# Kernel tuning notes

Measured on AMD Instinct MI355X. Metric: run time of the kernel, lower is better.

## Reference

```python
import jax, jax.numpy as jnp
import numpy as np

B, L, D, H, BS, R, MLP = 2, 4096, 768, 12, 64, 3, 3072
HD = D // H            # 64 head dim
NB = L // BS           # 64 blocks
EPS = 1e-6
SEED = 0               # connectivity_seed


def _rand_plan():
    """Static BigBird key-block plan for middle query blocks: [NB-2, 5+R].
    Columns: global first, global last, window (i-1, i, i+1), R random blocks."""
    rng = np.random.RandomState(SEED)
    rows = []
    for i in range(1, NB - 1):
        excl = {0, NB - 1, i - 1, i, i + 1}
        cand = np.array([j for j in range(NB) if j not in excl])
        rnd = rng.choice(cand, size=R, replace=False)
        rows.append(np.concatenate([np.array([0, NB - 1, i - 1, i, i + 1]), rnd]))
    return jnp.asarray(np.stack(rows), dtype=jnp.int32)

_PLAN = _rand_plan()


def _layernorm(x, scale, bias):
    mu = jnp.mean(x, axis=-1, keepdims=True)
    var = jnp.mean(jnp.square(x - mu), axis=-1, keepdims=True)
    return (x - mu) * jax.lax.rsqrt(var + EPS) * scale + bias


def _bigbird_attention(x, Wq, Wk, Wv, Wo):
    # projections: [B,L,D] x [D,H,HD] -> [B,H,L,HD]; flax scales q by 1/sqrt(HD)
    q = jnp.einsum('bld,dhk->bhlk', x, Wq) / jnp.sqrt(jnp.asarray(HD, x.dtype))
    k = jnp.einsum('bld,dhk->bhlk', x, Wk)
    v = jnp.einsum('bld,dhk->bhlk', x, Wv)
    qb = q.reshape(B, H, NB, BS, HD)
    kb = k.reshape(B, H, NB, BS, HD)
    vb = v.reshape(B, H, NB, BS, HD)
    # global query rows (first & last block) attend densely to all keys
    qg = qb[:, :, jnp.array([0, NB - 1])]                 # [B,H,2,BS,HD]
    sg = jnp.einsum('bhgqd,bhld->bhgql', qg, k)           # [B,H,2,BS,L]
    og = jnp.einsum('bhgql,bhld->bhgqd', jax.nn.softmax(sg, axis=-1), v)
    # middle query rows: gather window + global + random key blocks
    S = _PLAN.shape[1]                                     # 5 + R = 8 blocks
    km = kb[:, :, _PLAN].reshape(B, H, NB - 2, S * BS, HD)
    vm = vb[:, :, _PLAN].reshape(B, H, NB - 2, S * BS, HD)
    sm = jnp.einsum('bhmqd,bhmkd->bhmqk', qb[:, :, 1:NB - 1], km)
    om = jnp.einsum('bhmqk,bhmkd->bhmqd', jax.nn.softmax(sm, axis=-1), vm)
    ob = jnp.concatenate([og[:, :, :1], om, og[:, :, 1:]], axis=2)  # [B,H,NB,BS,HD]
    o = ob.reshape(B, H, L, HD)
    return jnp.einsum('bhlk,hkd->bld', o, Wo)


def setup_inputs() -> dict:
    key = jax.random.key(0)
    ks = jax.random.split(key, 8)
    s_qkv = (2.0 / (D + HD)) ** 0.5   # xavier-uniform-ish std
    s_mlp1 = (2.0 / (D + MLP)) ** 0.5
    return {
        'x': jax.random.normal(ks[0], (B, L, D), jnp.float32),
        'ln1_scale': jnp.ones((D,), jnp.float32),
        'ln1_bias': jnp.zeros((D,), jnp.float32),
        'Wq': jax.random.normal(ks[1], (D, H, HD), jnp.float32) * s_qkv,
        'Wk': jax.random.normal(ks[2], (D, H, HD), jnp.float32) * s_qkv,
        'Wv': jax.random.normal(ks[3], (D, H, HD), jnp.float32) * s_qkv,
        'Wo': jax.random.normal(ks[4], (H, HD, D), jnp.float32) * s_qkv,
        'ln2_scale': jnp.ones((D,), jnp.float32),
        'ln2_bias': jnp.zeros((D,), jnp.float32),
        'W1': jax.random.normal(ks[5], (D, MLP), jnp.float32) * s_mlp1,
        'b1': jnp.zeros((MLP,), jnp.float32),
        'W2': jax.random.normal(ks[6], (MLP, D), jnp.float32) * s_mlp1,
        'b2': jnp.zeros((D,), jnp.float32),
    }


def reference(x, ln1_scale, ln1_bias, Wq, Wk, Wv, Wo, ln2_scale, ln2_bias, W1, b1, W2, b2):
    h = _layernorm(x, ln1_scale, ln1_bias)
    attn = _bigbird_attention(h, Wq, Wk, Wv, Wo)
    x1 = attn + x                                  # residual (dropout deterministic)
    y = _layernorm(x1, ln2_scale, ln2_bias)
    y = jax.nn.relu(jnp.einsum('bld,df->blf', y, W1) + b1)
    y = jnp.einsum('blf,fd->bld', y, W2) + b2
    return x1 + y
```

## Files before the change

### kernel.cpp

```cpp
#include <hip/hip_runtime.h>
#include <stdint.h>

constexpr int D_MODEL = 768;
constexpr int SEQ     = 4096;
constexpr int NHEAD   = 12;
constexpr int HDIM    = 64;
constexpr int BATCH   = 2;
constexpr int DFF     = 3072;
constexpr int ROWS    = BATCH * SEQ;

typedef __attribute__((ext_vector_type(8))) __bf16 bfrag;
typedef __attribute__((ext_vector_type(8))) short  s16x8;
typedef __attribute__((ext_vector_type(4))) float  f32x4;

#define MFMA16(a, b, c) __builtin_amdgcn_mfma_f32_16x16x32_bf16((a), (b), (c), 0, 0, 0)
#define AS1(p) ((__attribute__((address_space(1))) void*)(uintptr_t)(p))
#define AS3(p) ((__attribute__((address_space(3))) void*)(p))

__device__ __forceinline__ float b2f(short s) {
  union { unsigned u; float f; } c;
  c.u = ((unsigned)(unsigned short)s) << 16;
  return c.f;
}
__device__ __forceinline__ short f2b(float f) {
  union { float f; unsigned u; } c;
  c.f = f;
  unsigned r = c.u + 0x7fffu + ((c.u >> 16) & 1u);
  return (short)(r >> 16);
}

struct PlanT { int v[64][8]; };

struct MTRng {
  unsigned mt[624];
  int mti;
  constexpr MTRng() : mt{}, mti(624) {
    mt[0] = 0u;
    for (int i = 1; i < 624; ++i)
      mt[i] = 1812433253u * (mt[i-1] ^ (mt[i-1] >> 30)) + (unsigned)i;
  }
  constexpr unsigned next() {
    if (mti >= 624) {
      for (int i = 0; i < 624; ++i) {
        unsigned y = (mt[i] & 0x80000000u) | (mt[(i+1) % 624] & 0x7fffffffu);
        unsigned v = mt[(i+397) % 624] ^ (y >> 1);
        if (y & 1u) v ^= 0x9908b0dfu;
        mt[i] = v;
      }
      mti = 0;
    }
    unsigned y = mt[mti++];
    y ^= y >> 11;
    y ^= (y << 7)  & 0x9d2c5680u;
    y ^= (y << 15) & 0xefc60000u;
    y ^= y >> 18;
    return y;
  }
  constexpr unsigned interval(unsigned mx) {
    unsigned mask = mx;
    mask |= mask >> 1; mask |= mask >> 2; mask |= mask >> 4;
    mask |= mask >> 8; mask |= mask >> 16;
    unsigned v = next() & mask;
    while (v > mx) v = next() & mask;
    return v;
  }
};

constexpr PlanT make_plan() {
  PlanT P{};
  MTRng rng{};
  for (int i = 1; i <= 62; ++i) {
    int cand[64] = {}; int n = 0;
    for (int j = 0; j < 64; ++j) {
      if (j == 0 || j == 63 || j == i-1 || j == i || j == i+1) continue;
      cand[n++] = j;
    }
    int perm[64] = {};
    for (int p = 0; p < n; ++p) perm[p] = p;
    for (int p = n - 1; p > 0; --p) {
      int j = (int)rng.interval((unsigned)p);
      int t = perm[p]; perm[p] = perm[j]; perm[j] = t;
    }
    P.v[i][0] = 0;  P.v[i][1] = 63; P.v[i][2] = i-1; P.v[i][3] = i; P.v[i][4] = i+1;
    P.v[i][5] = cand[perm[0]]; P.v[i][6] = cand[perm[1]]; P.v[i][7] = cand[perm[2]];
  }
  return P;
}
constexpr PlanT h_plan = make_plan();
__constant__ PlanT g_plan = h_plan;

__global__ __launch_bounds__(256) void ln_kernel(
    const float* __restrict__ x, const float* __restrict__ sc,
    const float* __restrict__ bi, short* __restrict__ y)
{
  const int row = blockIdx.x, tid = threadIdx.x;
  const size_t base = (size_t)row * D_MODEL;
  float v0 = x[base + tid], v1 = x[base + tid + 256], v2 = x[base + tid + 512];
  float s  = v0 + v1 + v2;
  float s2 = v0*v0 + v1*v1 + v2*v2;
  for (int off = 1; off < 64; off <<= 1) {
    s  += __shfl_xor(s,  off);
    s2 += __shfl_xor(s2, off);
  }
  __shared__ float red[8];
  if ((tid & 63) == 0) { red[tid >> 6] = s; red[4 + (tid >> 6)] = s2; }
  __syncthreads();
  s  = red[0] + red[1] + red[2] + red[3];
  s2 = red[4] + red[5] + red[6] + red[7];
  const float mu  = s * (1.f / 768.f);
  const float var = s2 * (1.f / 768.f) - mu * mu;
  const float rs  = rsqrtf(var + 1e-6f);
  short* yr = y + base;
  yr[tid]       = f2b((v0 - mu) * rs * sc[tid]       + bi[tid]);
  yr[tid + 256] = f2b((v1 - mu) * rs * sc[tid + 256] + bi[tid + 256]);
  yr[tid + 512] = f2b((v2 - mu) * rs * sc[tid + 512] + bi[tid + 512]);
}

struct TrArgs { const float* src[6]; short* dst[6]; };

__global__ __launch_bounds__(256) void tr_all(TrArgs a) {
  __shared__ short tile[32][33];
  const int idx = blockIdx.x;
  int w, bx, by, Rr, Cc;
  if (idx < 2304)      { w = idx / 576; int t = idx % 576;  bx = t % 24; by = t / 24; Rr = 768;  Cc = 768;  }
  else if (idx < 4608) { w = 4;         int t = idx - 2304; bx = t % 96; by = t / 96; Rr = 768;  Cc = 3072; }
  else                 { w = 5;         int t = idx - 4608; bx = t % 24; by = t / 24; Rr = 3072; Cc = 768;  }
  const float* in = a.src[w];
  short* out = a.dst[w];
  const int x0 = bx * 32, y0 = by * 32;
  const int tx = threadIdx.x & 31, ty = threadIdx.x >> 5;
  for (int i = 0; i < 32; i += 8)
    tile[ty + i][tx] = f2b(in[(size_t)(y0 + ty + i) * Cc + x0 + tx]);
  __syncthreads();
  for (int i = 0; i < 32; i += 8)
    out[(size_t)(x0 + ty + i) * Rr + y0 + tx] = tile[tx][ty + i];
}

enum { M_QKV = 0, M_RES = 3, M_BRELU = 4, M_BRES = 5 };

template <int MODE, int TN>
__global__ __launch_bounds__(256) void gemm_bt(
    const short* __restrict__ A, const short* __restrict__ Bt,
    void* __restrict__ Cv, short* __restrict__ C2, short* __restrict__ C3,
    const float* __restrict__ res, const float* __restrict__ bias, int N, int K)
{
  constexpr int NT = TN / 32;
  alignas(16) __shared__ short As[128 * 32];
  alignas(16) __shared__ short Bs[TN * 32];
  const int tid = threadIdx.x;
  const int wave = tid >> 6, lane = tid & 63;
  const int quad = lane >> 4, l15 = lane & 15;
  const int m0 = blockIdx.x * 128, n0 = blockIdx.y * TN;
  const int mw = (wave & 1) * 64, nw = (wave >> 1) * (TN / 2);

  f32x4 acc[4][NT];
#pragma unroll
  for (int i = 0; i < 4; ++i)
#pragma unroll
    for (int j = 0; j < NT; ++j) acc[i][j] = f32x4{0.f, 0.f, 0.f, 0.f};

  const int srow = wave * 32 + (lane >> 2);
  const int scol = (lane & 3) * 8;
  const size_t arow = (size_t)(m0 + srow) * K + scol;
  const size_t brow128 = (size_t)(n0 + srow) * K + scol;
  const size_t brow64  = (size_t)(n0 + wave * 16 + (lane >> 2)) * K + scol;

  for (int k0 = 0; k0 < K; k0 += 32) {
    __syncthreads();
    __builtin_amdgcn_global_load_lds(AS1(A + arow + k0),                AS3(As + (wave*32     ) * 32), 16, 0, 0);
    __builtin_amdgcn_global_load_lds(AS1(A + arow + k0 + (size_t)16*K), AS3(As + (wave*32 + 16) * 32), 16, 0, 0);
    if constexpr (TN == 128) {
      __builtin_amdgcn_global_load_lds(AS1(Bt + brow128 + k0),                AS3(Bs + (wave*32     ) * 32), 16, 0, 0);
      __builtin_amdgcn_global_load_lds(AS1(Bt + brow128 + k0 + (size_t)16*K), AS3(Bs + (wave*32 + 16) * 32), 16, 0, 0);
    } else {
      __builtin_amdgcn_global_load_lds(AS1(Bt + brow64 + k0), AS3(Bs + (wave*16) * 32), 16, 0, 0);
    }
    __syncthreads();
    bfrag af[4], bfv[NT];
#pragma unroll
    for (int mt = 0; mt < 4; ++mt)  af[mt]  = *(const bfrag*)(As + (mw + mt*16 + l15) * 32 + quad * 8);
#pragma unroll
    for (int nt = 0; nt < NT; ++nt) bfv[nt] = *(const bfrag*)(Bs + (nw + nt*16 + l15) * 32 + quad * 8);
#pragma unroll
    for (int mt = 0; mt < 4; ++mt)
#pragma unroll
      for (int nt = 0; nt < NT; ++nt)
        acc[mt][nt] = MFMA16(af[mt], bfv[nt], acc[mt][nt]);
  }

#pragma unroll
  for (int mt = 0; mt < 4; ++mt) {
#pragma unroll
    for (int nt = 0; nt < NT; ++nt) {
#pragma unroll
      for (int r = 0; r < 4; ++r) {
        const int gm = m0 + mw + mt*16 + quad*4 + r;
        const int gn = n0 + nw + nt*16 + l15;
        float v = acc[mt][nt][r];
        if (MODE == M_QKV) {
          const int seg = gn / 768, gn2 = gn - seg * 768;
          if (seg == 0)      ((short*)Cv)[(size_t)gm * 768 + gn2] = f2b(v * 0.125f);
          else if (seg == 1) C2[(size_t)gm * 768 + gn2] = f2b(v);
          else {
            const int bb = gm >> 12, l = gm & 4095, hh = gn2 >> 6, hd = gn2 & 63;
            C3[(((size_t)(bb * NHEAD + hh)) * HDIM + hd) * SEQ + l] = f2b(v);
          }
        } else {
          const size_t ci = (size_t)gm * N + gn;
          if (MODE == M_RES)   { ((float*)Cv)[ci] = v + res[ci]; }
          if (MODE == M_BRELU) { v += bias[gn]; ((short*)Cv)[ci] = f2b(v > 0.f ? v : 0.f); }
          if (MODE == M_BRES)  { ((float*)Cv)[ci] = v + bias[gn] + res[ci]; }
        }
      }
    }
  }
}

constexpr int PSTR = 72;
constexpr int KSTR = 68;

__global__ __launch_bounds__(256, 3) void attn_kernel(
    const short* __restrict__ q, const short* __restrict__ k,
    const short* __restrict__ vt, short* __restrict__ o,
    short* __restrict__ Opart, float* __restrict__ ml)
{
  alignas(16) __shared__ short KV[4][64 * KSTR];
  alignas(16) __shared__ short Pbuf[4][2 * 16 * PSTR];
  const int xi = blockIdx.x, h = blockIdx.y, b = blockIdx.z;
  const int tid = threadIdx.x, wave = tid >> 6, lane = tid & 63;
  const int quad = lane >> 4, l15 = lane & 15;
  const int r8 = lane >> 3, g8 = lane & 7;

  int qb, part = 0, g = 0;
  bool partial;
  if (xi < 62) { qb = xi + 1; partial = false; }
  else { const int t = xi - 62; g = t >> 3; part = t & 7; qb = g ? 63 : 0; partial = true; }

  const short* qp = q + (size_t)(b * SEQ + qb * 64 + wave * 16 + l15) * D_MODEL + h * HDIM;
  const bfrag qf0 = *(const bfrag*)(qp + quad * 8);
  const bfrag qf1 = *(const bfrag*)(qp + 32 + quad * 8);

  const short* kb_base = k  + (size_t)b * SEQ * D_MODEL + h * HDIM;
  const short* vt_base = vt + ((size_t)(b * NHEAD + h)) * HDIM * SEQ;

  const int sr0 = wave * 16 + r8, sr1 = wave * 16 + 8 + r8;

  auto kidx = [&](int t, int which) -> int {
    const int tt = t > 3 ? 3 : t;
    return partial ? (part * 8 + 2 * tt + which) : g_plan.v[qb][2 * tt + which];
  };
  auto load8 = [&](int k0i, int k1i, s16x8* R) {
    const short* ka = kb_base + (size_t)k0i * 64 * D_MODEL + g8 * 8;
    const short* kbp = kb_base + (size_t)k1i * 64 * D_MODEL + g8 * 8;
    const short* va = vt_base + (size_t)k0i * 64 + g8 * 8;
    const short* vb = vt_base + (size_t)k1i * 64 + g8 * 8;
    R[0] = *(const s16x8*)(ka  + (size_t)sr0 * D_MODEL);
    R[1] = *(const s16x8*)(ka  + (size_t)sr1 * D_MODEL);
    R[2] = *(const s16x8*)(kbp + (size_t)sr0 * D_MODEL);
    R[3] = *(const s16x8*)(kbp + (size_t)sr1 * D_MODEL);
    R[4] = *(const s16x8*)(va  + (size_t)sr0 * SEQ);
    R[5] = *(const s16x8*)(va  + (size_t)sr1 * SEQ);
    R[6] = *(const s16x8*)(vb  + (size_t)sr0 * SEQ);
    R[7] = *(const s16x8*)(vb  + (size_t)sr1 * SEQ);
  };

  float m_r[4], l_r[4];
  f32x4 oacc[4];
#pragma unroll
  for (int r = 0; r < 4; ++r) { m_r[r] = -1e9f; l_r[r] = 0.f; }
#pragma unroll
  for (int nt = 0; nt < 4; ++nt) oacc[nt] = f32x4{0.f, 0.f, 0.f, 0.f};

  short* pb = &Pbuf[wave][0];

  s16x8 R[8];
  load8(kidx(0, 0), kidx(0, 1), R);

  for (int it = 0; it < 4; ++it) {
    __syncthreads();
#pragma unroll
    for (int bu = 0; bu < 4; ++bu) {
      *(s16x8*)(&KV[bu][sr0 * KSTR + g8 * 8]) = R[2 * bu];
      *(s16x8*)(&KV[bu][sr1 * KSTR + g8 * 8]) = R[2 * bu + 1];
    }
    __syncthreads();

    load8(kidx(it + 1, 0), kidx(it + 1, 1), R);

    f32x4 s0[4], s1[4];
#pragma unroll
    for (int nt = 0; nt < 4; ++nt) {
      const int fr = (nt * 16 + l15) * KSTR + quad * 8;
      const bfrag ka0 = *(const bfrag*)(&KV[0][fr]);
      const bfrag ka1 = *(const bfrag*)(&KV[0][fr + 32]);
      const bfrag kb0 = *(const bfrag*)(&KV[1][fr]);
      const bfrag kb1 = *(const bfrag*)(&KV[1][fr + 32]);
      s0[nt] = f32x4{0.f,0.f,0.f,0.f}; s1[nt] = f32x4{0.f,0.f,0.f,0.f};
      s0[nt] = MFMA16(qf0, ka0, s0[nt]); s0[nt] = MFMA16(qf1, ka1, s0[nt]);
      s1[nt] = MFMA16(qf0, kb0, s1[nt]); s1[nt] = MFMA16(qf1, kb1, s1[nt]);
    }

    float alpha[4];
#pragma unroll
    for (int r = 0; r < 4; ++r) {
      float v = fmaxf(fmaxf(fmaxf(s0[0][r], s0[1][r]), fmaxf(s0[2][r], s0[3][r])),
                      fmaxf(fmaxf(s1[0][r], s1[1][r]), fmaxf(s1[2][r], s1[3][r])));
      v = fmaxf(v, __shfl_xor(v, 1));
      v = fmaxf(v, __shfl_xor(v, 2));
      v = fmaxf(v, __shfl_xor(v, 4));
      v = fmaxf(v, __shfl_xor(v, 8));
      const float mn = fmaxf(m_r[r], v);
      alpha[r] = __expf(m_r[r] - mn);
      m_r[r] = mn;
    }
    float psum[4] = {0.f, 0.f, 0.f, 0.f};
#pragma unroll
    for (int nt = 0; nt < 4; ++nt)
#pragma unroll
      for (int r = 0; r < 4; ++r) {
        const float p0 = __expf(s0[nt][r] - m_r[r]);
        const float p1 = __expf(s1[nt][r] - m_r[r]);
        s0[nt][r] = p0; s1[nt][r] = p1;
        psum[r] += p0 + p1;
      }
#pragma unroll
    for (int r = 0; r < 4; ++r) {
      float v = psum[r];
      v += __shfl_xor(v, 1); v += __shfl_xor(v, 2);
      v += __shfl_xor(v, 4); v += __shfl_xor(v, 8);
      l_r[r] = l_r[r] * alpha[r] + v;
    }

#pragma unroll
    for (int nt = 0; nt < 4; ++nt)
#pragma unroll
      for (int r = 0; r < 4; ++r) {
        pb[(quad * 4 + r) * PSTR + nt * 16 + l15]             = f2b(s0[nt][r]);
        pb[16 * PSTR + (quad * 4 + r) * PSTR + nt * 16 + l15] = f2b(s1[nt][r]);
      }

#pragma unroll
    for (int nt = 0; nt < 4; ++nt)
#pragma unroll
      for (int r = 0; r < 4; ++r) oacc[nt][r] *= alpha[r];
#pragma unroll
    for (int s = 0; s < 2; ++s) {
      const bfrag pf0 = *(const bfrag*)(pb + l15 * PSTR + s * 32 + quad * 8);
      const bfrag pf1 = *(const bfrag*)(pb + 16 * PSTR + l15 * PSTR + s * 32 + quad * 8);
#pragma unroll
      for (int nt = 0; nt < 4; ++nt) {
        const int fr = (nt * 16 + l15) * KSTR + s * 32 + quad * 8;
        const bfrag vf0 = *(const bfrag*)(&KV[2][fr]);
        const bfrag vf1 = *(const bfrag*)(&KV[3][fr]);
        oacc[nt] = MFMA16(pf0, vf0, oacc[nt]);
        oacc[nt] = MFMA16(pf1, vf1, oacc[nt]);
      }
    }
  }

  if (!partial) {
    short* op = o + (size_t)(b * SEQ + qb * 64 + wave * 16) * D_MODEL + h * HDIM;
#pragma unroll
    for (int r = 0; r < 4; ++r) {
      const float inv = 1.f / l_r[r];
#pragma unroll
      for (int nt = 0; nt < 4; ++nt)
        op[(size_t)(quad * 4 + r) * D_MODEL + nt * 16 + l15] = f2b(oacc[nt][r] * inv);
    }
  } else {
    const int pi = ((b * NHEAD + h) * 2 + g) * 8 + part;
    short* Op = Opart + (size_t)pi * 4096;
    float* mp = ml + (size_t)pi * 128;
#pragma unroll
    for (int r = 0; r < 4; ++r) {
      const int row = wave * 16 + quad * 4 + r;
#pragma unroll
      for (int nt = 0; nt < 4; ++nt)
        Op[row * 64 + nt * 16 + l15] = f2b(oacc[nt][r]);
      if (l15 == 0) { mp[row] = m_r[r]; mp[64 + row] = l_r[r]; }
    }
  }
}

__global__ __launch_bounds__(256) void attn_merge(
    const short* __restrict__ Opart, const float* __restrict__ ml,
    short* __restrict__ o)
{
  const int bi = blockIdx.x;
  const int g = bi & 1, h = (bi >> 1) % NHEAD, b = bi / (2 * NHEAD);
  const int qb = g ? 63 : 0;
  const int pi0 = bi * 8;
#pragma unroll
  for (int e = 0; e < 16; ++e) {
    const int idx = threadIdx.x + e * 256;
    const int r = idx >> 6, c = idx & 63;
    float ms = -1e9f;
#pragma unroll
    for (int p = 0; p < 8; ++p) ms = fmaxf(ms, ml[(size_t)(pi0 + p) * 128 + r]);
    float lsum = 0.f, osum = 0.f;
#pragma unroll
    for (int p = 0; p < 8; ++p) {
      const float w = __expf(ml[(size_t)(pi0 + p) * 128 + r] - ms);
      lsum += w * ml[(size_t)(pi0 + p) * 128 + 64 + r];
      osum += w * b2f(Opart[(size_t)(pi0 + p) * 4096 + idx]);
    }
    o[(size_t)(b * SEQ + qb * 64 + r) * D_MODEL + h * HDIM + c] = f2b(osum / lsum);
  }
}

extern "C" void kernel_launch(void* const* d_in, const int* in_sizes, int n_in,
                              void* d_out, int out_size, void* d_ws, size_t ws_size,
                              hipStream_t stream) {
  (void)in_sizes; (void)n_in; (void)out_size; (void)ws_size;
  const float* x    = (const float*)d_in[0];
  const float* ln1s = (const float*)d_in[1];
  const float* ln1b = (const float*)d_in[2];
  const float* Wq   = (const float*)d_in[3];
  const float* Wk   = (const float*)d_in[4];
  const float* Wv   = (const float*)d_in[5];
  const float* Wo   = (const float*)d_in[6];
  const float* ln2s = (const float*)d_in[7];
  const float* ln2b = (const float*)d_in[8];
  const float* W1   = (const float*)d_in[9];
  const float* b1   = (const float*)d_in[10];
  const float* W2   = (const float*)d_in[11];
  const float* b2   = (const float*)d_in[12];
  float* out = (float*)d_out;

  short* WqT  = (short*)((char*)d_ws + 256);
  short* WkT  = WqT  + 768 * 768;
  short* WvT  = WkT  + 768 * 768;
  short* WoT  = WvT  + 768 * 768;
  short* W1T  = WoT  + 768 * 768;
  short* W2T  = W1T  + (size_t)3072 * 768;
  short* hbuf = W2T  + (size_t)3072 * 768;
  short* qbuf = hbuf + (size_t)ROWS * D_MODEL;
  short* kbuf = qbuf + (size_t)ROWS * D_MODEL;
  short* vtb  = kbuf + (size_t)ROWS * D_MODEL;
  short* obuf = vtb  + (size_t)ROWS * D_MODEL;
  short* tbuf = qbuf;
  short* Opart = hbuf;
  float* mlbuf = (float*)(hbuf + (size_t)384 * 4096);

  TrArgs ta;
  ta.src[0] = Wq; ta.src[1] = Wk; ta.src[2] = Wv; ta.src[3] = Wo; ta.src[4] = W1; ta.src[5] = W2;
  ta.dst[0] = WqT; ta.dst[1] = WkT; ta.dst[2] = WvT; ta.dst[3] = WoT; ta.dst[4] = W1T; ta.dst[5] = W2T;
  tr_all<<<6912, 256, 0, stream>>>(ta);

  ln_kernel<<<ROWS, 256, 0, stream>>>(x, ln1s, ln1b, hbuf);

  gemm_bt<M_QKV, 128><<<dim3(64, 18), 256, 0, stream>>>(hbuf, WqT, qbuf, kbuf, vtb, nullptr, nullptr, 2304, 768);

  attn_kernel<<<dim3(78, 12, 2), 256, 0, stream>>>(qbuf, kbuf, vtb, obuf, Opart, mlbuf);
  attn_merge<<<48, 256, 0, stream>>>(Opart, mlbuf, obuf);

  gemm_bt<M_RES, 64><<<dim3(64, 12), 256, 0, stream>>>(obuf, WoT, out, nullptr, nullptr, x, nullptr, 768, 768);

  ln_kernel<<<ROWS, 256, 0, stream>>>(out, ln2s, ln2b, hbuf);

  gemm_bt<M_BRELU, 128><<<dim3(64, 24), 256, 0, stream>>>(hbuf, W1T, tbuf, nullptr, nullptr, nullptr, b1, 3072, 768);
  gemm_bt<M_BRES, 64> <<<dim3(64, 12), 256, 0, stream>>>(tbuf, W2T, out, nullptr, nullptr, out, b2, 768, 3072);
}
```

Baseline: 392.9 us.

## Replace GEMMs with 256x256 multi-stage pipelined kernel and split-K atomic FFN2

```diff
diff --git a/kernel.cpp b/kernel.cpp
--- a/kernel.cpp
+++ b/kernel.cpp
@@ -27,6 +27,15 @@
   c.f = f;
   unsigned r = c.u + 0x7fffu + ((c.u >> 16) & 1u);
   return (short)(r >> 16);
+}
+
+__device__ __forceinline__ void atomAddF(float* p, float v) {
+#if __has_builtin(__builtin_amdgcn_global_atomic_fadd_f32)
+  (void)__builtin_amdgcn_global_atomic_fadd_f32(
+      (__attribute__((address_space(1))) float*)(uintptr_t)p, v);
+#else
+  atomicAdd(p, v);
+#endif
 }
 
 struct PlanT { int v[64][8]; };
@@ -136,68 +145,129 @@
     out[(size_t)(x0 + ty + i) * Rr + y0 + tx] = tile[tx][ty + i];
 }
 
-enum { M_QKV = 0, M_RES = 3, M_BRELU = 4, M_BRES = 5 };
-
-template <int MODE, int TN>
-__global__ __launch_bounds__(256) void gemm_bt(
+enum { M_QKV = 0, M_RES = 3, M_BRELU = 4, M_BRES_AT = 6 };
+
+template <int MODE>
+__global__ __launch_bounds__(512, 2) void gemm256(
     const short* __restrict__ A, const short* __restrict__ Bt,
     void* __restrict__ Cv, short* __restrict__ C2, short* __restrict__ C3,
-    const float* __restrict__ res, const float* __restrict__ bias, int N, int K)
+    const float* __restrict__ res, const float* __restrict__ bias,
+    int N, int K, int ksz)
 {
-  constexpr int NT = TN / 32;
-  alignas(16) __shared__ short As[128 * 32];
-  alignas(16) __shared__ short Bs[TN * 32];
-  const int tid = threadIdx.x;
-  const int wave = tid >> 6, lane = tid & 63;
+  alignas(16) __shared__ short KV[10 * 8192];
+  const int tid  = threadIdx.x;
+  const int wid  = tid >> 6, lane = tid & 63;
   const int quad = lane >> 4, l15 = lane & 15;
-  const int m0 = blockIdx.x * 128, n0 = blockIdx.y * TN;
-  const int mw = (wave & 1) * 64, nw = (wave >> 1) * (TN / 2);
-
-  f32x4 acc[4][NT];
-#pragma unroll
-  for (int i = 0; i < 4; ++i)
-#pragma unroll
-    for (int j = 0; j < NT; ++j) acc[i][j] = f32x4{0.f, 0.f, 0.f, 0.f};
-
-  const int srow = wave * 32 + (lane >> 2);
-  const int scol = (lane & 3) * 8;
-  const size_t arow = (size_t)(m0 + srow) * K + scol;
-  const size_t brow128 = (size_t)(n0 + srow) * K + scol;
-  const size_t brow64  = (size_t)(n0 + wave * 16 + (lane >> 2)) * K + scol;
-
-  for (int k0 = 0; k0 < K; k0 += 32) {
-    __syncthreads();
-    __builtin_amdgcn_global_load_lds(AS1(A + arow + k0),                AS3(As + (wave*32     ) * 32), 16, 0, 0);
-    __builtin_amdgcn_global_load_lds(AS1(A + arow + k0 + (size_t)16*K), AS3(As + (wave*32 + 16) * 32), 16, 0, 0);
-    if constexpr (TN == 128) {
-      __builtin_amdgcn_global_load_lds(AS1(Bt + brow128 + k0),                AS3(Bs + (wave*32     ) * 32), 16, 0, 0);
-      __builtin_amdgcn_global_load_lds(AS1(Bt + brow128 + k0 + (size_t)16*K), AS3(Bs + (wave*32 + 16) * 32), 16, 0, 0);
-    } else {
-      __builtin_amdgcn_global_load_lds(AS1(Bt + brow64 + k0), AS3(Bs + (wave*16) * 32), 16, 0, 0);
-    }
-    __syncthreads();
-    bfrag af[4], bfv[NT];
-#pragma unroll
-    for (int mt = 0; mt < 4; ++mt)  af[mt]  = *(const bfrag*)(As + (mw + mt*16 + l15) * 32 + quad * 8);
-#pragma unroll
-    for (int nt = 0; nt < NT; ++nt) bfv[nt] = *(const bfrag*)(Bs + (nw + nt*16 + l15) * 32 + quad * 8);
-#pragma unroll
-    for (int mt = 0; mt < 4; ++mt)
-#pragma unroll
-      for (int nt = 0; nt < NT; ++nt)
-        acc[mt][nt] = MFMA16(af[mt], bfv[nt], acc[mt][nt]);
-  }
-
-#pragma unroll
-  for (int mt = 0; mt < 4; ++mt) {
-#pragma unroll
-    for (int nt = 0; nt < NT; ++nt) {
+  const int wr = wid >> 2, wn = wid & 3, bh = wn >> 1;
+  const int m0 = blockIdx.x * 256, n0 = blockIdx.y * 256;
+  const int kbase = blockIdx.z * ksz;
+  const int NK = ksz >> 6;
+
+  const int rsub = tid >> 3;
+  const int scol = ((tid & 7) ^ (rsub & 7)) * 8;
+  const short* pa  = A  + (size_t)(m0 + rsub) * K + kbase + scol;
+  const short* pb  = Bt + (size_t)(n0 + rsub) * K + kbase + scol;
+  const short* pa1 = pa + (size_t)128 * K;
+  const short* pb1 = pb + (size_t)128 * K;
+
+#define STAGE(slot, src) do {                                                       \
+    short* _d = (short*)KV + (slot) * 8192 + wid * 512;                             \
+    __builtin_amdgcn_global_load_lds(AS1(src), AS3(_d), 16, 0, 0);                  \
+    __builtin_amdgcn_global_load_lds(AS1((src) + (size_t)64 * K), AS3(_d + 4096), 16, 0, 0); \
+  } while (0)
+
+  const int xorv  = (l15 & 7) << 4;
+  const int aoff0 = l15 * 128 + ((quad * 16) ^ xorv);
+  const int aoff1 = l15 * 128 + ((64 + quad * 16) ^ xorv);
+  const int boff0 = (wn & 1) * 8192 + aoff0;
+  const int boff1 = (wn & 1) * 8192 + aoff1;
+
+  f32x4 acc[8][4];
+#pragma unroll
+  for (int i = 0; i < 8; ++i)
+#pragma unroll
+    for (int j = 0; j < 4; ++j) acc[i][j] = f32x4{0.f, 0.f, 0.f, 0.f};
+
+  STAGE(0, pa);       STAGE(1, pa1);
+  STAGE(2, pb);       STAGE(3, pb1);
+  STAGE(4, pa + 64);  STAGE(5, pa1 + 64);
+  asm volatile("s_waitcnt vmcnt(4)" ::: "memory");
+  __builtin_amdgcn_s_barrier();
+  __builtin_amdgcn_sched_barrier(0);
+
+#define LDA(mtb) _Pragma("unroll")                                   \
+    for (int mi = 0; mi < 4; ++mi) {                                 \
+      af[mi][0] = *(const bfrag*)(Ab0 + ((mtb) + mi) * 2048);        \
+      af[mi][1] = *(const bfrag*)(Ab1 + ((mtb) + mi) * 2048); }
+#define LDB(ntb) _Pragma("unroll")                                   \
+    for (int ni = 0; ni < 2; ++ni) {                                 \
+      bf[ni][0] = *(const bfrag*)(Bb0 + ((ntb) + ni) * 2048);        \
+      bf[ni][1] = *(const bfrag*)(Bb1 + ((ntb) + ni) * 2048); }
+#define MM(mtb, ntb)                                                 \
+    __builtin_amdgcn_s_setprio(1);                                   \
+    _Pragma("unroll")                                                \
+    for (int mi = 0; mi < 4; ++mi)                                   \
+      _Pragma("unroll")                                              \
+      for (int ni = 0; ni < 2; ++ni) {                               \
+        acc[(mtb)+mi][(ntb)+ni] = MFMA16(af[mi][0], bf[ni][0], acc[(mtb)+mi][(ntb)+ni]); \
+        acc[(mtb)+mi][(ntb)+ni] = MFMA16(af[mi][1], bf[ni][1], acc[(mtb)+mi][(ntb)+ni]); \
+      }                                                              \
+    __builtin_amdgcn_s_setprio(0);
+
+  int s0 = 0;
+  for (int kt = 0; kt < NK; ++kt) {
+    int tA = s0 + wr;      const int sA = (tA >= 10) ? tA - 10 : tA;
+    int tB = s0 + 2 + bh;  const int sB = (tB >= 10) ? tB - 10 : tB;
+    const char* KB  = (const char*)KV;
+    const char* Ab0 = KB + sA * 16384 + aoff0;
+    const char* Ab1 = KB + sA * 16384 + aoff1;
+    const char* Bb0 = KB + sB * 16384 + boff0;
+    const char* Bb1 = KB + sB * 16384 + boff1;
+    int st0 = s0 + 6; if (st0 >= 10) st0 -= 10;
+    int st1 = st0 + 1; if (st1 >= 10) st1 -= 10;
+    int st2 = st1 + 1; if (st2 >= 10) st2 -= 10;
+    int st3 = st2 + 1; if (st3 >= 10) st3 -= 10;
+    int kkB = kt + 1; if (kkB >= NK) kkB = 0;
+    int kkA = kt + 2; if (kkA >= NK) kkA = 0;
+
+    bfrag af[4][2], bf[2][2];
+
+    LDB(0); LDA(0);
+    STAGE(st0, pb + kkB * 64);
+    MM(0, 0);
+    __builtin_amdgcn_sched_barrier(0);
+    LDB(2);
+    STAGE(st1, pb1 + kkB * 64);
+    MM(0, 2);
+    __builtin_amdgcn_sched_barrier(0);
+    LDA(4);
+    STAGE(st2, pa + kkA * 64);
+    MM(4, 2);
+    __builtin_amdgcn_sched_barrier(0);
+    LDB(0);
+    STAGE(st3, pa1 + kkA * 64);
+    MM(4, 0);
+    asm volatile("s_waitcnt vmcnt(4)" ::: "memory");
+    __builtin_amdgcn_s_barrier();
+    __builtin_amdgcn_sched_barrier(0);
+
+    s0 += 4; if (s0 >= 10) s0 -= 10;
+  }
+#undef LDA
+#undef LDB
+#undef MM
+#undef STAGE
+
+#pragma unroll
+  for (int mt = 0; mt < 8; ++mt) {
+#pragma unroll
+    for (int nt = 0; nt < 4; ++nt) {
 #pragma unroll
       for (int r = 0; r < 4; ++r) {
-        const int gm = m0 + mw + mt*16 + quad*4 + r;
-        const int gn = n0 + nw + nt*16 + l15;
+        const int gm = m0 + wr * 128 + mt * 16 + quad * 4 + r;
+        const int gn = n0 + wn * 64 + nt * 16 + l15;
         float v = acc[mt][nt][r];
-        if (MODE == M_QKV) {
+        if constexpr (MODE == M_QKV) {
           const int seg = gn / 768, gn2 = gn - seg * 768;
           if (seg == 0)      ((short*)Cv)[(size_t)gm * 768 + gn2] = f2b(v * 0.125f);
           else if (seg == 1) C2[(size_t)gm * 768 + gn2] = f2b(v);
@@ -205,11 +275,16 @@
             const int bb = gm >> 12, l = gm & 4095, hh = gn2 >> 6, hd = gn2 & 63;
             C3[(((size_t)(bb * NHEAD + hh)) * HDIM + hd) * SEQ + l] = f2b(v);
           }
+        } else if constexpr (MODE == M_RES) {
+          const size_t ci = (size_t)gm * N + gn;
+          ((float*)Cv)[ci] = v + res[ci];
+        } else if constexpr (MODE == M_BRELU) {
+          const size_t ci = (size_t)gm * N + gn;
+          v += bias[gn];
+          ((short*)Cv)[ci] = f2b(v > 0.f ? v : 0.f);
         } else {
           const size_t ci = (size_t)gm * N + gn;
-          if (MODE == M_RES)   { ((float*)Cv)[ci] = v + res[ci]; }
-          if (MODE == M_BRELU) { v += bias[gn]; ((short*)Cv)[ci] = f2b(v > 0.f ? v : 0.f); }
-          if (MODE == M_BRES)  { ((float*)Cv)[ci] = v + bias[gn] + res[ci]; }
+          atomAddF((float*)Cv + ci, v + 0.5f * bias[gn]);
         }
       }
     }
@@ -449,15 +524,20 @@
 
   ln_kernel<<<ROWS, 256, 0, stream>>>(x, ln1s, ln1b, hbuf);
 
-  gemm_bt<M_QKV, 128><<<dim3(64, 18), 256, 0, stream>>>(hbuf, WqT, qbuf, kbuf, vtb, nullptr, nullptr, 2304, 768);
+  gemm256<M_QKV><<<dim3(32, 9), 512, 0, stream>>>(
+      hbuf, WqT, qbuf, kbuf, vtb, nullptr, nullptr, 2304, 768, 768);
 
   attn_kernel<<<dim3(78, 12, 2), 256, 0, stream>>>(qbuf, kbuf, vtb, obuf, Opart, mlbuf);
   attn_merge<<<48, 256, 0, stream>>>(Opart, mlbuf, obuf);
 
-  gemm_bt<M_RES, 64><<<dim3(64, 12), 256, 0, stream>>>(obuf, WoT, out, nullptr, nullptr, x, nullptr, 768, 768);
+  gemm256<M_RES><<<dim3(32, 3), 512, 0, stream>>>(
+      obuf, WoT, out, nullptr, nullptr, x, nullptr, 768, 768, 768);
 
   ln_kernel<<<ROWS, 256, 0, stream>>>(out, ln2s, ln2b, hbuf);
 
-  gemm_bt<M_BRELU, 128><<<dim3(64, 24), 256, 0, stream>>>(hbuf, W1T, tbuf, nullptr, nullptr, nullptr, b1, 3072, 768);
-  gemm_bt<M_BRES, 64> <<<dim3(64, 12), 256, 0, stream>>>(tbuf, W2T, out, nullptr, nullptr, out, b2, 768, 3072);
-}
+  gemm256<M_BRELU><<<dim3(32, 12), 512, 0, stream>>>(
+      hbuf, W1T, tbuf, nullptr, nullptr, nullptr, b1, 3072, 768, 768);
+
+  gemm256<M_BRES_AT><<<dim3(32, 3, 2), 512, 0, stream>>>(
+      tbuf, W2T, out, nullptr, nullptr, nullptr, b2, 768, 3072, 1536);
+}
```

After: 402.9 us. 2.6% more time.

## Triple-buffer GEMM LDS staging with async prefetch and vectorize V-transpose stores

Applied to the files above, without the earlier changes.

```diff
diff --git a/kernel.cpp b/kernel.cpp
--- a/kernel.cpp
+++ b/kernel.cpp
@@ -11,6 +11,7 @@
 
 typedef __attribute__((ext_vector_type(8))) __bf16 bfrag;
 typedef __attribute__((ext_vector_type(8))) short  s16x8;
+typedef __attribute__((ext_vector_type(4))) short  s16x4;
 typedef __attribute__((ext_vector_type(4))) float  f32x4;
 
 #define MFMA16(a, b, c) __builtin_amdgcn_mfma_f32_16x16x32_bf16((a), (b), (c), 0, 0, 0)
@@ -145,8 +146,8 @@
     const float* __restrict__ res, const float* __restrict__ bias, int N, int K)
 {
   constexpr int NT = TN / 32;
-  alignas(16) __shared__ short As[128 * 32];
-  alignas(16) __shared__ short Bs[TN * 32];
+  alignas(16) __shared__ short As[3][128 * 32];
+  alignas(16) __shared__ short Bs[3][TN * 32];
   const int tid = threadIdx.x;
   const int wave = tid >> 6, lane = tid & 63;
   const int quad = lane >> 4, l15 = lane & 15;
@@ -165,47 +166,75 @@
   const size_t brow128 = (size_t)(n0 + srow) * K + scol;
   const size_t brow64  = (size_t)(n0 + wave * 16 + (lane >> 2)) * K + scol;
 
+  auto STAGE = [&](int buf, int k0) {
+    __builtin_amdgcn_global_load_lds(AS1(A + arow + k0),                AS3(As[buf] + (wave*32     ) * 32), 16, 0, 0);
+    __builtin_amdgcn_global_load_lds(AS1(A + arow + k0 + (size_t)16*K), AS3(As[buf] + (wave*32 + 16) * 32), 16, 0, 0);
+    if constexpr (TN == 128) {
+      __builtin_amdgcn_global_load_lds(AS1(Bt + brow128 + k0),                AS3(Bs[buf] + (wave*32     ) * 32), 16, 0, 0);
+      __builtin_amdgcn_global_load_lds(AS1(Bt + brow128 + k0 + (size_t)16*K), AS3(Bs[buf] + (wave*32 + 16) * 32), 16, 0, 0);
+    } else {
+      __builtin_amdgcn_global_load_lds(AS1(Bt + brow64 + k0), AS3(Bs[buf] + (wave*16) * 32), 16, 0, 0);
+    }
+  };
+
+  STAGE(0, 0);
+  STAGE(1, 32);
+
+  int cb = 0;
   for (int k0 = 0; k0 < K; k0 += 32) {
-    __syncthreads();
-    __builtin_amdgcn_global_load_lds(AS1(A + arow + k0),                AS3(As + (wave*32     ) * 32), 16, 0, 0);
-    __builtin_amdgcn_global_load_lds(AS1(A + arow + k0 + (size_t)16*K), AS3(As + (wave*32 + 16) * 32), 16, 0, 0);
-    if constexpr (TN == 128) {
-      __builtin_amdgcn_global_load_lds(AS1(Bt + brow128 + k0),                AS3(Bs + (wave*32     ) * 32), 16, 0, 0);
-      __builtin_amdgcn_global_load_lds(AS1(Bt + brow128 + k0 + (size_t)16*K), AS3(Bs + (wave*32 + 16) * 32), 16, 0, 0);
-    } else {
-      __builtin_amdgcn_global_load_lds(AS1(Bt + brow64 + k0), AS3(Bs + (wave*16) * 32), 16, 0, 0);
-    }
-    __syncthreads();
+    const int kn = k0 + 64;
+    int sb = cb + 2; if (sb >= 3) sb -= 3;
+    STAGE(sb, kn < K ? kn : 0);
+    if constexpr (TN == 128) asm volatile("s_waitcnt vmcnt(8)" ::: "memory");
+    else                     asm volatile("s_waitcnt vmcnt(6)" ::: "memory");
+    __builtin_amdgcn_s_barrier();
+    __builtin_amdgcn_sched_barrier(0);
+
     bfrag af[4], bfv[NT];
 #pragma unroll
-    for (int mt = 0; mt < 4; ++mt)  af[mt]  = *(const bfrag*)(As + (mw + mt*16 + l15) * 32 + quad * 8);
-#pragma unroll
-    for (int nt = 0; nt < NT; ++nt) bfv[nt] = *(const bfrag*)(Bs + (nw + nt*16 + l15) * 32 + quad * 8);
+    for (int mt = 0; mt < 4; ++mt)  af[mt]  = *(const bfrag*)(As[cb] + (mw + mt*16 + l15) * 32 + quad * 8);
+#pragma unroll
+    for (int nt = 0; nt < NT; ++nt) bfv[nt] = *(const bfrag*)(Bs[cb] + (nw + nt*16 + l15) * 32 + quad * 8);
 #pragma unroll
     for (int mt = 0; mt < 4; ++mt)
 #pragma unroll
       for (int nt = 0; nt < NT; ++nt)
         acc[mt][nt] = MFMA16(af[mt], bfv[nt], acc[mt][nt]);
-  }
+
+    asm volatile("s_waitcnt lgkmcnt(0)" ::: "memory");
+    __builtin_amdgcn_sched_barrier(0);
+    __builtin_amdgcn_s_barrier();
+    cb = cb + 1; if (cb >= 3) cb = 0;
+  }
+  asm volatile("s_waitcnt vmcnt(0)" ::: "memory");
 
 #pragma unroll
   for (int mt = 0; mt < 4; ++mt) {
 #pragma unroll
     for (int nt = 0; nt < NT; ++nt) {
-#pragma unroll
-      for (int r = 0; r < 4; ++r) {
-        const int gm = m0 + mw + mt*16 + quad*4 + r;
+      if (MODE == M_QKV) {
         const int gn = n0 + nw + nt*16 + l15;
-        float v = acc[mt][nt][r];
-        if (MODE == M_QKV) {
-          const int seg = gn / 768, gn2 = gn - seg * 768;
-          if (seg == 0)      ((short*)Cv)[(size_t)gm * 768 + gn2] = f2b(v * 0.125f);
-          else if (seg == 1) C2[(size_t)gm * 768 + gn2] = f2b(v);
-          else {
-            const int bb = gm >> 12, l = gm & 4095, hh = gn2 >> 6, hd = gn2 & 63;
-            C3[(((size_t)(bb * NHEAD + hh)) * HDIM + hd) * SEQ + l] = f2b(v);
+        const int seg = gn / 768, gn2 = gn - seg * 768;
+        const int gm0 = m0 + mw + mt*16 + quad*4;
+        if (seg == 2) {
+          const int bb = gm0 >> 12, l = gm0 & 4095, hh = gn2 >> 6, hd = gn2 & 63;
+          s16x4 pk{f2b(acc[mt][nt][0]), f2b(acc[mt][nt][1]),
+                   f2b(acc[mt][nt][2]), f2b(acc[mt][nt][3])};
+          *(s16x4*)(&C3[(((size_t)(bb * NHEAD + hh)) * HDIM + hd) * SEQ + l]) = pk;
+        } else {
+#pragma unroll
+          for (int r = 0; r < 4; ++r) {
+            const float v = acc[mt][nt][r];
+            if (seg == 0) ((short*)Cv)[(size_t)(gm0 + r) * 768 + gn2] = f2b(v * 0.125f);
+            else          C2[(size_t)(gm0 + r) * 768 + gn2] = f2b(v);
           }
-        } else {
+        }
+      } else {
+#pragma unroll
+        for (int r = 0; r < 4; ++r) {
+          const int gm = m0 + mw + mt*16 + quad*4 + r;
+          const int gn = n0 + nw + nt*16 + l15;
+          float v = acc[mt][nt][r];
           const size_t ci = (size_t)gm * N + gn;
           if (MODE == M_RES)   { ((float*)Cv)[ci] = v + res[ci]; }
           if (MODE == M_BRELU) { v += bias[gn]; ((short*)Cv)[ci] = f2b(v > 0.f ? v : 0.f); }
```

Result: faster. 367.7 us (-6.4%).
